# Kernel tuning notes

Measured on AMD Instinct MI355X. Metric: run time of the kernel, lower is better.

The kernel has to match this reference:

```python
import jax, jax.numpy as jnp
import numpy as np

C = 256      # d_model
H = 8        # nhead
DF = 1024    # dim_feedforward
LE = 2048    # ego tokens
LA = 2048    # other-agent tokens
N_MATCH = 1024


def setup_inputs() -> dict:
    key = jax.random.key(0)
    ks = jax.random.split(key, 16)
    def rn(k, shape, s=0.02):
        return jax.random.normal(k, shape, dtype=jnp.float32) * s
    inp = {}
    inp['x_ego'] = jax.random.normal(ks[0], (LE, C), dtype=jnp.float32)
    inp['x_agent'] = jax.random.normal(ks[1], (LA, C), dtype=jnp.float32)
    # query_fusion MLP(2C -> C -> C -> C), torch Linear weight is (out, in)
    inp['Wf1'] = rn(ks[2], (C, 2 * C)); inp['bf1'] = jnp.zeros((C,), jnp.float32)
    inp['Wf2'] = rn(ks[3], (C, C));     inp['bf2'] = jnp.zeros((C,), jnp.float32)
    inp['Wf3'] = rn(ks[4], (C, C));     inp['bf3'] = jnp.zeros((C,), jnp.float32)
    # nn.MultiheadAttention packed in-proj and out-proj
    inp['Wqkv'] = rn(ks[5], (3 * C, C)); inp['bqkv'] = jnp.zeros((3 * C,), jnp.float32)
    inp['Wo'] = rn(ks[6], (C, C));       inp['bo'] = jnp.zeros((C,), jnp.float32)
    # FFN
    inp['W1'] = rn(ks[7], (DF, C)); inp['b1'] = jnp.zeros((DF,), jnp.float32)
    inp['W2'] = rn(ks[8], (C, DF)); inp['b2'] = jnp.zeros((C,), jnp.float32)
    # LayerNorms
    inp['g1'] = jnp.ones((C,), jnp.float32); inp['be1'] = jnp.zeros((C,), jnp.float32)
    inp['g2'] = jnp.ones((C,), jnp.float32); inp['be2'] = jnp.zeros((C,), jnp.float32)
    # unique 1D positions: first N_MATCH agent positions overlap ego, rest don't
    inp['pos_ego'] = jnp.arange(LE, dtype=jnp.int32)
    pa = np.concatenate([np.arange(N_MATCH), np.arange(LA - N_MATCH) + 10_000_000])
    inp['pos_agent'] = jnp.asarray(pa, dtype=jnp.int32)
    inp['n_remain'] = LA - N_MATCH  # static python int
    return inp


def _ln(t, g, b):
    m = t.mean(-1, keepdims=True)
    v = t.var(-1, keepdims=True)
    return (t - m) / jnp.sqrt(v + 1e-5) * g + b


def reference(x_ego, x_agent, Wf1, bf1, Wf2, bf2, Wf3, bf3, Wqkv, bqkv, Wo, bo,
              W1, b1, W2, b2, g1, be1, g2, be2, pos_ego, pos_agent, n_remain):
    # ---- position-keyed grouping / fuse (replaces the host-side dict loop) ----
    eq = pos_agent[:, None] == pos_ego[None, :]          # [La, Le]
    matched_e = eq.any(axis=0)                           # ego token has same-pos agent token
    agent_for_ego = jnp.argmax(eq, axis=0)               # [Le] matching agent index (valid where matched)
    fused_in = jnp.concatenate([x_ego, x_agent[agent_for_ego]], axis=-1)  # [Le, 2C]
    h = jax.nn.relu(fused_in @ Wf1.T + bf1)
    h = jax.nn.relu(h @ Wf2.T + bf2)
    fused = h @ Wf3.T + bf3                              # query_fusion MLP output [Le, C]
    ego_out = jnp.where(matched_e[:, None], fused, x_ego)
    # agent tokens with no ego match, in original agent order (fixed count n_remain)
    remain_idx = jnp.nonzero(~eq.any(axis=1), size=n_remain)[0]
    q = jnp.concatenate([ego_out, x_agent[remain_idx]], axis=0)[None]  # (1, Lq, C)
    kv = jnp.concatenate([x_ego, x_agent], axis=0)[None]               # (1, Lk, C)
    # ---- MultiheadAttention (batch_first, eval: dropout off) ----
    Wq, Wk, Wv = jnp.split(Wqkv, 3, axis=0)
    bq, bk, bv = jnp.split(bqkv, 3, axis=0)
    dh = C // H
    def heads(t, W, b):
        return (t @ W.T + b).reshape(1, -1, H, dh).transpose(0, 2, 1, 3)
    qh, kh, vh = heads(q, Wq, bq), heads(kv, Wk, bk), heads(kv, Wv, bv)
    scores = jnp.einsum('bhqd,bhkd->bhqk', qh, kh) / (float(dh) ** 0.5)
    attn = jax.nn.softmax(scores, axis=-1)
    o = jnp.einsum('bhqk,bhkd->bhqd', attn, vh).transpose(0, 2, 1, 3).reshape(1, -1, C)
    o = o @ Wo.T + bo
    # ---- residual + norm1 + FFN + residual + norm2 ----
    yq = _ln(q + o, g1, be1)
    ff = jax.nn.relu(yq @ W1.T + b1) @ W2.T + b2
    return _ln(yq + ff, g2, be2)
```

## Files before the change

### kernel.cpp

```cpp
#include <hip/hip_runtime.h>


#define LE 2048
#define LA 2048
#define CDIM 256
#define HN 8
#define DH 32
#define DFF 1024
#define NREM 1024
#define LQC 3072
#define LKC 4096
#define KSPLIT 4
#define NIT (LKC / KSPLIT / 64)

typedef unsigned short u16;
typedef unsigned int u32;
typedef __attribute__((ext_vector_type(8))) short bf16x8;
typedef __attribute__((ext_vector_type(4))) float f32x4;

__device__ __forceinline__ u32 pk_bf16(float a, float b) {
    u32 ua = (__builtin_bit_cast(u32, a) + 0x8000u) >> 16;
    u32 ub = (__builtin_bit_cast(u32, b) + 0x8000u) >> 16;
    return ua | (ub << 16);
}
__device__ __forceinline__ u16 bf16_1(float a) {
    return (u16)((__builtin_bit_cast(u32, a) + 0x8000u) >> 16);
}
__device__ __forceinline__ float fast_exp2(float x) {
    return __builtin_amdgcn_exp2f(x);
}

__global__ __launch_bounds__(256) void k_prep(const int* __restrict__ pos_ego,
                                              const int* __restrict__ pos_agent,
                                              const float* __restrict__ x_ego,
                                              const float* __restrict__ x_agent,
                                              int* __restrict__ afe,
                                              int* __restrict__ matched,
                                              int* __restrict__ unmatched,
                                              u16* __restrict__ kv_b) {
    __shared__ int ps[2048];
    int b = blockIdx.x;
    if (b < 8) {
        for (int i = threadIdx.x; i < LA; i += 256) ps[i] = pos_agent[i];
        __syncthreads();
        int e = b * 256 + threadIdx.x;
        int pe = pos_ego[e];
        int idx = 0, found = 0;
#pragma unroll 8
        for (int a = 0; a < LA; ++a) {
            int eq = (ps[a] == pe);
            if (eq && !found) { idx = a; found = 1; }
        }
        afe[e] = idx;
        matched[e] = found;
    } else if (b < 16) {
        for (int i = threadIdx.x; i < LE; i += 256) ps[i] = pos_ego[i];
        __syncthreads();
        int a = (b - 8) * 256 + threadIdx.x;
        int pav = pos_agent[a];
        int found = 0;
#pragma unroll 8
        for (int e = 0; e < LE; ++e) found |= (ps[e] == pav);
        unmatched[a] = !found;
    } else {
        int t = (b - 16) * 256 + threadIdx.x;
        int j = t >> 5, c8 = t & 31;
        const float* src = (j < LE) ? (x_ego + (size_t)j * CDIM)
                                    : (x_agent + (size_t)(j - LE) * CDIM);
        float4 f0 = *(const float4*)(src + c8 * 8);
        float4 f1 = *(const float4*)(src + c8 * 8 + 4);
        uint4 o;
        o.x = pk_bf16(f0.x, f0.y); o.y = pk_bf16(f0.z, f0.w);
        o.z = pk_bf16(f1.x, f1.y); o.w = pk_bf16(f1.z, f1.w);
        *(uint4*)(kv_b + (size_t)j * CDIM + c8 * 8) = o;
    }
}

struct WPtrs { const float* p[7]; };
__constant__ __device__ const int woff[8] = {0, 131072, 196608, 262144,
                                             458752, 524288, 786432, 1048576};

__global__ __launch_bounds__(256) void k_stage2(const int* __restrict__ unmatched,
                                                int* __restrict__ remain,
                                                const int* __restrict__ afe,
                                                const float* __restrict__ x_ego,
                                                const float* __restrict__ x_agent,
                                                u16* __restrict__ fused_b,
                                                WPtrs wp, u16* __restrict__ wb) {
    int b = blockIdx.x;
    if (b == 0) {
        __shared__ int s[256];
        int t = threadIdx.x;
        int base_i = t * 8;
        int flags[8];
        int cnt = 0;
#pragma unroll
        for (int j = 0; j < 8; ++j) { flags[j] = unmatched[base_i + j]; cnt += flags[j]; }
        s[t] = cnt;
        __syncthreads();
        for (int off = 1; off < 256; off <<= 1) {
            int v = (t >= off) ? s[t - off] : 0;
            __syncthreads();
            s[t] += v;
            __syncthreads();
        }
        int pos = s[t] - cnt;
#pragma unroll
        for (int j = 0; j < 8; ++j) {
            if (flags[j]) {
                if (pos < NREM) remain[pos] = base_i + j;
                pos++;
            }
        }
    } else if (b <= 512) {
        int t = (b - 1) * 256 + threadIdx.x;
        int e = t >> 6, c8 = t & 63;
        const float* src;
        int col;
        if (c8 < 32) { src = x_ego + (size_t)e * CDIM; col = c8 * 8; }
        else { src = x_agent + (size_t)afe[e] * CDIM; col = (c8 - 32) * 8; }
        float4 f0 = *(const float4*)(src + col);
        float4 f1 = *(const float4*)(src + col + 4);
        uint4 o;
        o.x = pk_bf16(f0.x, f0.y); o.y = pk_bf16(f0.z, f0.w);
        o.z = pk_bf16(f1.x, f1.y); o.w = pk_bf16(f1.z, f1.w);
        *(uint4*)(fused_b + (size_t)e * 512 + c8 * 8) = o;
    } else {
        int g = ((b - 513) * 256 + threadIdx.x) * 8;
        int s = 0;
#pragma unroll
        for (int i = 1; i < 7; ++i) s += (g >= woff[i]);
        const float* src = wp.p[s] + (g - woff[s]);
        float4 f0 = *(const float4*)(src);
        float4 f1 = *(const float4*)(src + 4);
        uint4 o;
        o.x = pk_bf16(f0.x, f0.y); o.y = pk_bf16(f0.z, f0.w);
        o.z = pk_bf16(f1.x, f1.y); o.w = pk_bf16(f1.z, f1.w);
        *(uint4*)(wb + g) = o;
    }
}

__global__ __launch_bounds__(256) void k_finalize_q(const int* __restrict__ matched,
                                                    const int* __restrict__ remain,
                                                    const float* __restrict__ x_ego,
                                                    const float* __restrict__ x_agent,
                                                    float* __restrict__ qbuf,
                                                    u16* __restrict__ qbuf_b) {
    int t = blockIdx.x * 256 + threadIdx.x;
    int row = t >> 5, c8 = t & 31;
    const float* src;
    if (row < LE) {
        src = matched[row] ? (qbuf + (size_t)row * CDIM) : (x_ego + (size_t)row * CDIM);
    } else {
        int idx = remain[row - LE];
        idx = min(max(idx, 0), LA - 1);
        src = x_agent + (size_t)idx * CDIM;
    }
    float4 f0 = *(const float4*)(src + c8 * 8);
    float4 f1 = *(const float4*)(src + c8 * 8 + 4);
    float* dst = qbuf + (size_t)row * CDIM + c8 * 8;
    *(float4*)(dst) = f0;
    *(float4*)(dst + 4) = f1;
    uint4 o;
    o.x = pk_bf16(f0.x, f0.y); o.y = pk_bf16(f0.z, f0.w);
    o.z = pk_bf16(f1.x, f1.y); o.w = pk_bf16(f1.z, f1.w);
    *(uint4*)(qbuf_b + (size_t)row * CDIM + c8 * 8) = o;
}

template <int EPI, bool RELU>
__global__ __launch_bounds__(256) void gemm_bf16(const u16* __restrict__ A,
                                                 const u16* __restrict__ B,
                                                 const float* __restrict__ bias,
                                                 void* __restrict__ C,
                                                 int M, int N, int K) {
    const int tid = threadIdx.x;
    const int w = tid >> 6, lane = tid & 63;
    const int quad = lane >> 4, qi = lane & 15;
    const int wm = w >> 1, wn = w & 1;
    const int bm = blockIdx.y * 64, bn = blockIdx.x * 64;

    const u16* pa0 = A + (size_t)(bm + wm * 32 + qi) * K + quad * 8;
    const u16* pa1 = pa0 + (size_t)16 * K;
    const u16* pb0 = B + (size_t)(bn + wn * 32 + qi) * K + quad * 8;
    const u16* pb1 = pb0 + (size_t)16 * K;

    f32x4 acc00 = {0.f, 0.f, 0.f, 0.f}, acc01 = {0.f, 0.f, 0.f, 0.f};
    f32x4 acc10 = {0.f, 0.f, 0.f, 0.f}, acc11 = {0.f, 0.f, 0.f, 0.f};

#pragma unroll 4
    for (int k = 0; k < K; k += 32) {
        bf16x8 a0 = *(const bf16x8*)(pa0 + k);
        bf16x8 a1 = *(const bf16x8*)(pa1 + k);
        bf16x8 b0 = *(const bf16x8*)(pb0 + k);
        bf16x8 b1 = *(const bf16x8*)(pb1 + k);
        acc00 = __builtin_amdgcn_mfma_f32_16x16x32_bf16(a0, b0, acc00, 0, 0, 0);
        acc01 = __builtin_amdgcn_mfma_f32_16x16x32_bf16(a0, b1, acc01, 0, 0, 0);
        acc10 = __builtin_amdgcn_mfma_f32_16x16x32_bf16(a1, b0, acc10, 0, 0, 0);
        acc11 = __builtin_amdgcn_mfma_f32_16x16x32_bf16(a1, b1, acc11, 0, 0, 0);
    }

#pragma unroll
    for (int i = 0; i < 2; ++i) {
#pragma unroll
        for (int j = 0; j < 2; ++j) {
            f32x4 acc = (i == 0) ? (j == 0 ? acc00 : acc01) : (j == 0 ? acc10 : acc11);
            int n = bn + wn * 32 + j * 16 + qi;
            int mbase = bm + wm * 32 + i * 16 + quad * 4;
            float bs = bias[n];
            float v[4];
#pragma unroll
            for (int r = 0; r < 4; ++r) {
                float x = acc[r] + bs;
                if (RELU) x = fmaxf(x, 0.f);
                v[r] = x;
            }
            if (EPI == 0) {
                float* Cf = (float*)C;
#pragma unroll
                for (int r = 0; r < 4; ++r) Cf[(size_t)(mbase + r) * N + n] = v[r];
            } else {
                u16* Cb = (u16*)C;
#pragma unroll
                for (int r = 0; r < 4; ++r) Cb[(size_t)(mbase + r) * N + n] = bf16_1(v[r]);
            }
        }
    }
}

__global__ __launch_bounds__(256) void k_qkv(const u16* __restrict__ qbuf_b,
                                             const u16* __restrict__ kv_b,
                                             const u16* __restrict__ Wq,
                                             const u16* __restrict__ Wkv,
                                             const float* __restrict__ bqkv,
                                             u16* __restrict__ qb,
                                             u16* __restrict__ kbp,
                                             u16* __restrict__ vtb,
                                             float qscale) {
    int b = blockIdx.x;
    const u16 *A, *B;
    const float* bias;
    int bm, bn, mode;
    if (b < 192) {
        A = qbuf_b; B = Wq; bias = bqkv;
        bm = (b >> 2) * 64; bn = (b & 3) * 64; mode = 0;
    } else {
        int c = b - 192;
        A = kv_b; B = Wkv; bias = bqkv + 256;
        bm = (c >> 3) * 64; bn = (c & 7) * 64; mode = 1;
    }
    const int tid = threadIdx.x;
    const int w = tid >> 6, lane = tid & 63;
    const int quad = lane >> 4, qi = lane & 15;
    const int wm = w >> 1, wn = w & 1;
    const int K = 256;

    const u16* pa0 = A + (size_t)(bm + wm * 32 + qi) * K + quad * 8;
    const u16* pa1 = pa0 + (size_t)16 * K;
    const u16* pb0 = B + (size_t)(bn + wn * 32 + qi) * K + quad * 8;
    const u16* pb1 = pb0 + (size_t)16 * K;

    f32x4 acc00 = {0.f, 0.f, 0.f, 0.f}, acc01 = {0.f, 0.f, 0.f, 0.f};
    f32x4 acc10 = {0.f, 0.f, 0.f, 0.f}, acc11 = {0.f, 0.f, 0.f, 0.f};
#pragma unroll 4
    for (int k = 0; k < 256; k += 32) {
        bf16x8 a0 = *(const bf16x8*)(pa0 + k);
        bf16x8 a1 = *(const bf16x8*)(pa1 + k);
        bf16x8 b0 = *(const bf16x8*)(pb0 + k);
        bf16x8 b1 = *(const bf16x8*)(pb1 + k);
        acc00 = __builtin_amdgcn_mfma_f32_16x16x32_bf16(a0, b0, acc00, 0, 0, 0);
        acc01 = __builtin_amdgcn_mfma_f32_16x16x32_bf16(a0, b1, acc01, 0, 0, 0);
        acc10 = __builtin_amdgcn_mfma_f32_16x16x32_bf16(a1, b0, acc10, 0, 0, 0);
        acc11 = __builtin_amdgcn_mfma_f32_16x16x32_bf16(a1, b1, acc11, 0, 0, 0);
    }
#pragma unroll
    for (int i = 0; i < 2; ++i) {
#pragma unroll
        for (int j = 0; j < 2; ++j) {
            f32x4 acc = (i == 0) ? (j == 0 ? acc00 : acc01) : (j == 0 ? acc10 : acc11);
            int n = bn + wn * 32 + j * 16 + qi;
            int mbase = bm + wm * 32 + i * 16 + quad * 4;
            float bs = bias[n];
            float v[4];
#pragma unroll
            for (int r = 0; r < 4; ++r) v[r] = acc[r] + bs;
            if (mode == 0) {
#pragma unroll
                for (int r = 0; r < 4; ++r)
                    qb[(size_t)(mbase + r) * 256 + n] = bf16_1(v[r] * qscale);
            } else if (n < 256) {
#pragma unroll
                for (int r = 0; r < 4; ++r)
                    kbp[(size_t)(mbase + r) * 256 + n] = bf16_1(v[r]);
            } else {
                ushort4 o4;
                o4.x = bf16_1(v[0]); o4.y = bf16_1(v[1]);
                o4.z = bf16_1(v[2]); o4.w = bf16_1(v[3]);
                *(ushort4*)(vtb + (size_t)(n - 256) * LKC + mbase) = o4;
            }
        }
    }
}

__global__ __launch_bounds__(256) void attn_mfma(const u16* __restrict__ qb,
                                                 const u16* __restrict__ kb,
                                                 const u16* __restrict__ vtb,
                                                 float* __restrict__ Pl,
                                                 float* __restrict__ Pacc) {
    __shared__ u16 Kt[2][64 * 32];
    __shared__ u16 Vt[2][32 * 64];
    __shared__ u16 plds[4][16 * 64];
    const int tid = threadIdx.x;
    const int w = tid >> 6, lane = tid & 63;
    const int quad = lane >> 4, qi = lane & 15;
    const int h = blockIdx.y, ks = blockIdx.z;
    const int q0 = blockIdx.x * 64 + w * 16;

    bf16x8 qf = *(const bf16x8*)(qb + (size_t)(q0 + qi) * CDIM + h * DH + quad * 8);

    f32x4 O0 = {0.f, 0.f, 0.f, 0.f}, O1 = {0.f, 0.f, 0.f, 0.f};
    float lsum = 0.f;

    const int krow = w * 16 + (lane >> 2), kcp = lane & 3;
    const int kc = kcp ^ (krow & 3);
    const u16* kg0 = kb + (size_t)krow * CDIM + h * DH + kc * 8;
    const int kdst = krow * 32 + kcp * 8;
    const int vd = w * 8 + (lane >> 3), vcp = lane & 7;
    const int vc = vcp ^ (vd & 7);
    const u16* vg0 = vtb + (size_t)(h * DH + vd) * LKC + vc * 8;
    const int vdst = vd * 64 + vcp * 8;

    const int ka0 = qi * 32 + ((quad ^ (qi & 3)) << 3);
    const int v00o = qi * 64 + ((quad ^ (qi & 7)) << 3);
    const int v01o = qi * 64 + (((quad + 4) ^ (qi & 7)) << 3);
    const int swz = (qi & 7);
    const int rd0 = qi * 64 + ((quad ^ swz) << 3);
    const int rd1 = qi * 64 + (((4 + quad) ^ swz) << 3);
    const int half = (quad & 1) << 2;

    int kt = ks * (LKC / KSPLIT);
    {
        bf16x8 kr = *(const bf16x8*)(kg0 + (size_t)kt * CDIM);
        bf16x8 vr = *(const bf16x8*)(vg0 + kt);
        *(bf16x8*)&Kt[0][kdst] = kr;
        *(bf16x8*)&Vt[0][vdst] = vr;
    }
    int buf = 0;
    for (int it = 0; it < NIT; ++it, kt += 64) {
        __syncthreads();
        bf16x8 knext, vnext;
        const bool more = (it + 1 < NIT);
        if (more) {
            knext = *(const bf16x8*)(kg0 + (size_t)(kt + 64) * CDIM);
            vnext = *(const bf16x8*)(vg0 + kt + 64);
        }

        bf16x8 a0 = *(const bf16x8*)&Kt[buf][ka0];
        bf16x8 a1 = *(const bf16x8*)&Kt[buf][ka0 + 16 * 32];
        bf16x8 a2 = *(const bf16x8*)&Kt[buf][ka0 + 32 * 32];
        bf16x8 a3 = *(const bf16x8*)&Kt[buf][ka0 + 48 * 32];
        f32x4 z = {0.f, 0.f, 0.f, 0.f};
        f32x4 s0 = __builtin_amdgcn_mfma_f32_16x16x32_bf16(a0, qf, z, 0, 0, 0);
        f32x4 s1 = __builtin_amdgcn_mfma_f32_16x16x32_bf16(a1, qf, z, 0, 0, 0);
        f32x4 s2 = __builtin_amdgcn_mfma_f32_16x16x32_bf16(a2, qf, z, 0, 0, 0);
        f32x4 s3 = __builtin_amdgcn_mfma_f32_16x16x32_bf16(a3, qf, z, 0, 0, 0);

        float p0[4], p1[4], p2[4], p3[4];
#pragma unroll
        for (int r = 0; r < 4; ++r) {
            p0[r] = fast_exp2(s0[r]); p1[r] = fast_exp2(s1[r]);
            p2[r] = fast_exp2(s2[r]); p3[r] = fast_exp2(s3[r]);
            lsum += p0[r] + p1[r] + p2[r] + p3[r];
        }

        u16* pb = &plds[w][0];
#pragma unroll
        for (int t = 0; t < 4; ++t) {
            int jg = t * 2 + (quad >> 1);
            int off = qi * 64 + ((jg ^ swz) << 3) + half;
            uint2 pw;
            float* pp = (t == 0) ? p0 : (t == 1) ? p1 : (t == 2) ? p2 : p3;
            pw.x = pk_bf16(pp[0], pp[1]);
            pw.y = pk_bf16(pp[2], pp[3]);
            *(uint2*)&pb[off] = pw;
        }
        bf16x8 pa0 = *(bf16x8*)&pb[rd0];
        bf16x8 pa1 = *(bf16x8*)&pb[rd1];

        bf16x8 v00 = *(const bf16x8*)&Vt[buf][v00o];
        bf16x8 v01 = *(const bf16x8*)&Vt[buf][v01o];
        bf16x8 v10 = *(const bf16x8*)&Vt[buf][v00o + 16 * 64];
        bf16x8 v11 = *(const bf16x8*)&Vt[buf][v01o + 16 * 64];
        O0 = __builtin_amdgcn_mfma_f32_16x16x32_bf16(pa0, v00, O0, 0, 0, 0);
        O0 = __builtin_amdgcn_mfma_f32_16x16x32_bf16(pa1, v01, O0, 0, 0, 0);
        O1 = __builtin_amdgcn_mfma_f32_16x16x32_bf16(pa0, v10, O1, 0, 0, 0);
        O1 = __builtin_amdgcn_mfma_f32_16x16x32_bf16(pa1, v11, O1, 0, 0, 0);

        if (more) {
            *(bf16x8*)&Kt[buf ^ 1][kdst] = knext;
            *(bf16x8*)&Vt[buf ^ 1][vdst] = vnext;
        }
        buf ^= 1;
    }

    lsum += __shfl_xor(lsum, 16, 64);
    lsum += __shfl_xor(lsum, 32, 64);

    int pbase = (h * KSPLIT + ks) * LQC + q0;
    if (quad == 0) Pl[pbase + qi] = lsum;
#pragma unroll
    for (int r = 0; r < 4; ++r) {
        int q = quad * 4 + r;
        float* pa = Pacc + (size_t)(pbase + q) * 32;
        pa[qi] = O0[r];
        pa[16 + qi] = O1[r];
    }
}

__global__ __launch_bounds__(256) void attn_combine(const float* __restrict__ Pl,
                                                    const float* __restrict__ Pacc,
                                                    u16* __restrict__ attn_b) {
    int t = blockIdx.x * 256 + threadIdx.x;
    int row = t >> 6;
    int h = (t >> 3) & 7;
    int d4 = t & 7;
    float L = 0.f;
    float o[4] = {};
#pragma unroll
    for (int ck = 0; ck < KSPLIT; ++ck) {
        size_t pidx = (size_t)(h * KSPLIT + ck) * LQC + row;
        L += Pl[pidx];
        float4 a = *(const float4*)(Pacc + pidx * 32 + d4 * 4);
        o[0] += a.x; o[1] += a.y; o[2] += a.z; o[3] += a.w;
    }
    float inv = 1.0f / L;
    ushort4 ov;
    ov.x = bf16_1(o[0] * inv); ov.y = bf16_1(o[1] * inv);
    ov.z = bf16_1(o[2] * inv); ov.w = bf16_1(o[3] * inv);
    *(ushort4*)(attn_b + (size_t)row * CDIM + h * DH + d4 * 4) = ov;
}

template <bool EMIT_BF16>
__global__ __launch_bounds__(256) void ln_kernel(const float* __restrict__ X,
                                                 const float* __restrict__ R,
                                                 const float* __restrict__ g,
                                                 const float* __restrict__ b,
                                                 float* __restrict__ out,
                                                 u16* __restrict__ out_b) {
    int lane = threadIdx.x & 63;
    int row = blockIdx.x * 4 + (threadIdx.x >> 6);
    const float* x = X + (size_t)row * CDIM;
    const float* r = R + (size_t)row * CDIM;
    float4 xv = *(const float4*)(x + lane * 4);
    float4 rv = *(const float4*)(r + lane * 4);
    float v[4] = {xv.x + rv.x, xv.y + rv.y, xv.z + rv.z, xv.w + rv.w};
    float s = v[0] + v[1] + v[2] + v[3];
    float sq = v[0] * v[0] + v[1] * v[1] + v[2] * v[2] + v[3] * v[3];
#pragma unroll
    for (int off = 32; off >= 1; off >>= 1) {
        s += __shfl_xor(s, off, 64);
        sq += __shfl_xor(sq, off, 64);
    }
    float mean = s * (1.f / 256.f);
    float var = sq * (1.f / 256.f) - mean * mean;
    float rstd = rsqrtf(var + 1e-5f);
    float4 gv = *(const float4*)(g + lane * 4);
    float4 bv = *(const float4*)(b + lane * 4);
    float4 o = make_float4((v[0] - mean) * rstd * gv.x + bv.x,
                           (v[1] - mean) * rstd * gv.y + bv.y,
                           (v[2] - mean) * rstd * gv.z + bv.z,
                           (v[3] - mean) * rstd * gv.w + bv.w);
    *(float4*)(out + (size_t)row * CDIM + lane * 4) = o;
    if (EMIT_BF16) {
        uint2 ob;
        ob.x = pk_bf16(o.x, o.y);
        ob.y = pk_bf16(o.z, o.w);
        *(uint2*)(out_b + (size_t)row * CDIM + lane * 4) = ob;
    }
}

extern "C" void kernel_launch(void* const* d_in, const int* in_sizes, int n_in,
                              void* d_out, int out_size, void* d_ws, size_t ws_size,
                              hipStream_t stream) {
    const float* x_ego = (const float*)d_in[0];
    const float* x_agent = (const float*)d_in[1];
    const float* Wf1 = (const float*)d_in[2];
    const float* bf1 = (const float*)d_in[3];
    const float* Wf2 = (const float*)d_in[4];
    const float* bf2 = (const float*)d_in[5];
    const float* Wf3 = (const float*)d_in[6];
    const float* bf3 = (const float*)d_in[7];
    const float* Wqkv = (const float*)d_in[8];
    const float* bqkv = (const float*)d_in[9];
    const float* Wo = (const float*)d_in[10];
    const float* bo = (const float*)d_in[11];
    const float* W1 = (const float*)d_in[12];
    const float* b1 = (const float*)d_in[13];
    const float* W2 = (const float*)d_in[14];
    const float* b2 = (const float*)d_in[15];
    const float* g1 = (const float*)d_in[16];
    const float* be1 = (const float*)d_in[17];
    const float* g2 = (const float*)d_in[18];
    const float* be2 = (const float*)d_in[19];
    const int* pos_ego = (const int*)d_in[20];
    const int* pos_agent = (const int*)d_in[21];

    float* ws = (float*)d_ws;
    size_t o = 0;
    float* qbuf = ws + o; o += 786432;
    float* o2 = ws + o; o += 786432;
    float* yq = ws + o; o += 786432;
    float* ff2 = ws + o; o += 786432;
    float* Pl = ws + o; o += HN * KSPLIT * LQC;
    float* Pacc = ws + o; o += (size_t)HN * KSPLIT * LQC * 32;
    u16* wb = (u16*)(ws + o); o += 524288;
    u16* fused_b = (u16*)(ws + o); o += 524288;
    u16* h1_b = (u16*)(ws + o); o += 262144;
    u16* h2_b = (u16*)(ws + o); o += 262144;
    u16* qbuf_b = (u16*)(ws + o); o += 393216;
    u16* kv_b = (u16*)(ws + o); o += 524288;
    u16* qb = (u16*)(ws + o); o += 393216;
    u16* kb = (u16*)(ws + o); o += 524288;
    u16* vtb = (u16*)(ws + o); o += 524288;
    u16* attn_b = (u16*)(ws + o); o += 393216;
    u16* ff1_b = (u16*)(ws + o); o += 1572864;
    u16* yq_b = (u16*)(ws + o); o += 393216;
    int* afe = (int*)(ws + o);
    int* matched = afe + LE;
    int* unmatched = matched + LE;
    int* remain = unmatched + LA;

    const u16* Wf1_b = wb + 0;
    const u16* Wf2_b = wb + 131072;
    const u16* Wf3_b = wb + 196608;
    const u16* Wq_b = wb + 262144;
    const u16* Wkv_b = wb + 327680;
    const u16* Wo_b = wb + 458752;
    const u16* W1_b = wb + 524288;
    const u16* W2_b = wb + 786432;

    k_prep<<<16 + (LKC * 32) / 256, 256, 0, stream>>>(pos_ego, pos_agent, x_ego, x_agent,
                                                      afe, matched, unmatched, kv_b);
    WPtrs wp;
    wp.p[0] = Wf1; wp.p[1] = Wf2; wp.p[2] = Wf3; wp.p[3] = Wqkv;
    wp.p[4] = Wo; wp.p[5] = W1; wp.p[6] = W2;
    k_stage2<<<1025, 256, 0, stream>>>(unmatched, remain, afe, x_ego, x_agent,
                                       fused_b, wp, wb);

    const float qscale = 0.17677669529663687f * 1.4426950408889634f;

    gemm_bf16<1, true><<<dim3(4, 32), 256, 0, stream>>>(fused_b, Wf1_b, bf1, h1_b,
                                                        LE, 256, 512);
    gemm_bf16<1, true><<<dim3(4, 32), 256, 0, stream>>>(h1_b, Wf2_b, bf2, h2_b,
                                                        LE, 256, 256);
    gemm_bf16<0, false><<<dim3(4, 32), 256, 0, stream>>>(h2_b, Wf3_b, bf3, qbuf,
                                                         LE, 256, 256);
    k_finalize_q<<<(LQC * 32) / 256, 256, 0, stream>>>(matched, remain, x_ego, x_agent,
                                                       qbuf, qbuf_b);

    k_qkv<<<704, 256, 0, stream>>>(qbuf_b, kv_b, Wq_b, Wkv_b, bqkv, qb, kb, vtb, qscale);

    attn_mfma<<<dim3(LQC / 64, HN, KSPLIT), 256, 0, stream>>>(qb, kb, vtb, Pl, Pacc);
    attn_combine<<<(LQC * 64) / 256, 256, 0, stream>>>(Pl, Pacc, attn_b);

    gemm_bf16<0, false><<<dim3(4, 48), 256, 0, stream>>>(attn_b, Wo_b, bo, o2,
                                                         LQC, 256, 256);
    ln_kernel<true><<<LQC / 4, 256, 0, stream>>>(qbuf, o2, g1, be1, yq, yq_b);

    gemm_bf16<1, true><<<dim3(16, 48), 256, 0, stream>>>(yq_b, W1_b, b1, ff1_b,
                                                         LQC, DFF, 256);
    gemm_bf16<0, false><<<dim3(4, 48), 256, 0, stream>>>(ff1_b, W2_b, b2, ff2,
                                                         LQC, 256, DFF);
    ln_kernel<false><<<LQC / 4, 256, 0, stream>>>(yq, ff2, g2, be2, (float*)d_out, nullptr);
}
```

Measured before the change: 260.6 us.

## Replace quadratic position matching with shared-memory hash table kernel

Replaces the all-pairs ego/agent position comparison with a single-block kernel. That kernel builds open-addressing hash tables in LDS with atomicCAS and then probes them, giving linear-time matching. The bf16 conversion of the key/value inputs is split into its own kernel. This removes the 2048-iteration scan per thread, but adds a separate kernel launch and serializes matching into one workgroup. It also relies on positions being unique and never equal to -1.

```diff
diff --git a/kernel.cpp b/kernel.cpp
--- a/kernel.cpp
+++ b/kernel.cpp
@@ -30,50 +30,77 @@
     return __builtin_amdgcn_exp2f(x);
 }
 
-__global__ __launch_bounds__(256) void k_prep(const int* __restrict__ pos_ego,
-                                              const int* __restrict__ pos_agent,
-                                              const float* __restrict__ x_ego,
+__global__ __launch_bounds__(1024) void k_match(const int* __restrict__ pos_ego,
+                                                const int* __restrict__ pos_agent,
+                                                int* __restrict__ afe,
+                                                int* __restrict__ matched,
+                                                int* __restrict__ unmatched) {
+    __shared__ int keyA[4096], valA[4096], keyE[4096];
+    const int t = threadIdx.x;
+#pragma unroll
+    for (int i = 0; i < 4; ++i) { keyA[t + i * 1024] = -1; keyE[t + i * 1024] = -1; }
+    __syncthreads();
+#pragma unroll
+    for (int i = 0; i < 2; ++i) {
+        int a = t + i * 1024;
+        int p = pos_agent[a];
+        u32 h = ((u32)p * 2654435761u) >> 20;
+        while (true) {
+            int prev = atomicCAS(&keyA[h], -1, p);
+            if (prev == -1) { valA[h] = a; break; }
+            h = (h + 1) & 4095;
+        }
+        int e = t + i * 1024;
+        int pe = pos_ego[e];
+        u32 he = ((u32)pe * 2654435761u) >> 20;
+        while (true) {
+            int prev = atomicCAS(&keyE[he], -1, pe);
+            if (prev == -1) break;
+            he = (he + 1) & 4095;
+        }
+    }
+    __syncthreads();
+#pragma unroll
+    for (int i = 0; i < 2; ++i) {
+        int e = t + i * 1024;
+        int p = pos_ego[e];
+        u32 h = ((u32)p * 2654435761u) >> 20;
+        int idx = 0, fnd = 0;
+        while (true) {
+            int k = keyA[h];
+            if (k == p) { idx = valA[h]; fnd = 1; break; }
+            if (k == -1) break;
+            h = (h + 1) & 4095;
+        }
+        afe[e] = idx;
+        matched[e] = fnd;
+        int a = t + i * 1024;
+        int pa_ = pos_agent[a];
+        u32 ha = ((u32)pa_ * 2654435761u) >> 20;
+        int fnd2 = 0;
+        while (true) {
+            int k = keyE[ha];
+            if (k == pa_) { fnd2 = 1; break; }
+            if (k == -1) break;
+            ha = (ha + 1) & 4095;
+        }
+        unmatched[a] = !fnd2;
+    }
+}
+
+__global__ __launch_bounds__(256) void k_prep(const float* __restrict__ x_ego,
                                               const float* __restrict__ x_agent,
-                                              int* __restrict__ afe,
-                                              int* __restrict__ matched,
-                                              int* __restrict__ unmatched,
                                               u16* __restrict__ kv_b) {
-    __shared__ int ps[2048];
-    int b = blockIdx.x;
-    if (b < 8) {
-        for (int i = threadIdx.x; i < LA; i += 256) ps[i] = pos_agent[i];
-        __syncthreads();
-        int e = b * 256 + threadIdx.x;
-        int pe = pos_ego[e];
-        int idx = 0, found = 0;
-#pragma unroll 8
-        for (int a = 0; a < LA; ++a) {
-            int eq = (ps[a] == pe);
-            if (eq && !found) { idx = a; found = 1; }
-        }
-        afe[e] = idx;
-        matched[e] = found;
-    } else if (b < 16) {
-        for (int i = threadIdx.x; i < LE; i += 256) ps[i] = pos_ego[i];
-        __syncthreads();
-        int a = (b - 8) * 256 + threadIdx.x;
-        int pav = pos_agent[a];
-        int found = 0;
-#pragma unroll 8
-        for (int e = 0; e < LE; ++e) found |= (ps[e] == pav);
-        unmatched[a] = !found;
-    } else {
-        int t = (b - 16) * 256 + threadIdx.x;
-        int j = t >> 5, c8 = t & 31;
-        const float* src = (j < LE) ? (x_ego + (size_t)j * CDIM)
-                                    : (x_agent + (size_t)(j - LE) * CDIM);
-        float4 f0 = *(const float4*)(src + c8 * 8);
-        float4 f1 = *(const float4*)(src + c8 * 8 + 4);
-        uint4 o;
-        o.x = pk_bf16(f0.x, f0.y); o.y = pk_bf16(f0.z, f0.w);
-        o.z = pk_bf16(f1.x, f1.y); o.w = pk_bf16(f1.z, f1.w);
-        *(uint4*)(kv_b + (size_t)j * CDIM + c8 * 8) = o;
-    }
+    int t = blockIdx.x * 256 + threadIdx.x;
+    int j = t >> 5, c8 = t & 31;
+    const float* src = (j < LE) ? (x_ego + (size_t)j * CDIM)
+                                : (x_agent + (size_t)(j - LE) * CDIM);
+    float4 f0 = *(const float4*)(src + c8 * 8);
+    float4 f1 = *(const float4*)(src + c8 * 8 + 4);
+    uint4 o;
+    o.x = pk_bf16(f0.x, f0.y); o.y = pk_bf16(f0.z, f0.w);
+    o.z = pk_bf16(f1.x, f1.y); o.w = pk_bf16(f1.z, f1.w);
+    *(uint4*)(kv_b + (size_t)j * CDIM + c8 * 8) = o;
 }
 
 struct WPtrs { const float* p[7]; };
@@ -538,8 +565,8 @@
     const u16* W1_b = wb + 524288;
     const u16* W2_b = wb + 786432;
 
-    k_prep<<<16 + (LKC * 32) / 256, 256, 0, stream>>>(pos_ego, pos_agent, x_ego, x_agent,
-                                                      afe, matched, unmatched, kv_b);
+    k_match<<<1, 1024, 0, stream>>>(pos_ego, pos_agent, afe, matched, unmatched);
+    k_prep<<<(LKC * 32) / 256, 256, 0, stream>>>(x_ego, x_agent, kv_b);
     WPtrs wp;
     wp.p[0] = Wf1; wp.p[1] = Wf2; wp.p[2] = Wf3; wp.p[3] = Wqkv;
     wp.p[4] = Wo; wp.p[5] = W1; wp.p[6] = W2;
```

Result: faster. 220.2 us (-15.5%).
